# Kernel optimization log

Measured on AMD Instinct MI355X. Metric: run time of the kernel, lower is better.

The kernel has to match this reference:

```python
import jax, jax.numpy as jnp
import numpy as np

B, S, D, H = 4, 2048, 2048, 8192  # batch, seq, d_model, hidden (power of 2 for FHT)


def fwht(x):
    """Fast Walsh-Hadamard transform along the last axis, normalized by 1/sqrt(n).

    Iterative butterfly: O(n log n). n must be a power of 2.
    """
    orig_shape = x.shape
    n = orig_shape[-1]
    x = x.reshape(-1, n)
    h = 1
    while h < n:
        # view as (rows, n/(2h) blocks, 2 halves, h) and do the butterfly
        xb = x.reshape(-1, n // (2 * h), 2, h)
        a = xb[:, :, 0, :]
        b = xb[:, :, 1, :]
        x = jnp.stack([a + b, a - b], axis=2).reshape(-1, n)
        h *= 2
    scale = jnp.asarray(1.0 / np.sqrt(n), dtype=x.dtype)
    return (x * scale).reshape(orig_shape)


def setup_inputs() -> dict:
    key = jax.random.key(0)
    kx, k1, k2, k3 = jax.random.split(key, 4)
    x = jax.random.normal(kx, (B, S, D), dtype=jnp.float32)
    # nn.Linear weights: [out_features, in_features], no bias (Llama FFN style)
    W1 = jax.random.normal(k1, (H, D), dtype=jnp.float32) * (1.0 / np.sqrt(D))
    W2 = jax.random.normal(k2, (D, H), dtype=jnp.float32) * (1.0 / np.sqrt(H))
    W3 = jax.random.normal(k3, (H, D), dtype=jnp.float32) * (1.0 / np.sqrt(D))
    return {"x": x, "W1": W1, "W2": W2, "W3": W3}


def reference(x, W1, W2, W3):
    # w2( fht( silu(w1(x)) * w3(x) ) )
    up_gate = jnp.einsum("bsd,hd->bsh", x, W1)          # w1(x): [B,S,H]
    up_lin = jnp.einsum("bsd,hd->bsh", x, W3)           # w3(x): [B,S,H]
    hidden = jax.nn.silu(up_gate) * up_lin              # SwiGLU gate
    hidden = fwht(hidden)                               # fast Hadamard transform over H
    out = jnp.einsum("bsh,dh->bsd", hidden, W2)         # w2(.): [B,S,D]
    return out
```

## Files before the change

### kernel.cpp

```cpp
#include <hip/hip_runtime.h>

typedef __attribute__((ext_vector_type(8))) __bf16 bf16x8;
typedef __attribute__((ext_vector_type(4))) float f32x4;

#define GLOAD_LDS16(g, l)                                                     \
  __builtin_amdgcn_global_load_lds(                                           \
      (const __attribute__((address_space(1))) void*)(g),                     \
      (__attribute__((address_space(3))) void*)(l), 16, 0, 0)

#define BAR() __builtin_amdgcn_s_barrier()
#define SB0() __builtin_amdgcn_sched_barrier(0)
#define LGKM(n)                                                               \
  do {                                                                        \
    asm volatile("s_waitcnt lgkmcnt(" #n ")" ::: "memory");                   \
    SB0();                                                                    \
  } while (0)
#define VMCNT0() asm volatile("s_waitcnt vmcnt(0)" ::: "memory")
#define PRIO1() __builtin_amdgcn_s_setprio(1)
#define PRIO0() __builtin_amdgcn_s_setprio(0)

__device__ __forceinline__ unsigned short f32_to_bf16(float f) {
  unsigned int u = __builtin_bit_cast(unsigned int, f);
  u += 0x7FFFu + ((u >> 16) & 1u);
  return (unsigned short)(u >> 16);
}

__global__ void conv_f32_bf16(const float* __restrict__ in,
                              unsigned short* __restrict__ out, int n4) {
  int stride = gridDim.x * blockDim.x;
  for (int i = blockIdx.x * blockDim.x + threadIdx.x; i < n4; i += stride) {
    float4 v = reinterpret_cast<const float4*>(in)[i];
    ushort4 o;
    o.x = f32_to_bf16(v.x);
    o.y = f32_to_bf16(v.y);
    o.z = f32_to_bf16(v.z);
    o.w = f32_to_bf16(v.w);
    reinterpret_cast<ushort4*>(out)[i] = o;
  }
}

__global__ void fwht_rows_bf16(const float* __restrict__ in,
                               unsigned short* __restrict__ out) {
  __shared__ float s[8192];
  const int tid = threadIdx.x;
  const float* row = in + (size_t)blockIdx.x * 8192;
#pragma unroll
  for (int i = 0; i < 8; ++i)
    reinterpret_cast<float4*>(s)[tid + i * 256] =
        reinterpret_cast<const float4*>(row)[tid + i * 256];
  for (int h = 1; h < 8192; h <<= 1) {
    __syncthreads();
#pragma unroll
    for (int it = 0; it < 16; ++it) {
      int i = tid + it * 256;
      int j = ((i & ~(h - 1)) << 1) | (i & (h - 1));
      float a = s[j], b = s[j + h];
      s[j] = a + b;
      s[j + h] = a - b;
    }
  }
  __syncthreads();
  const float scale = 0.011048543456039806f;
  unsigned short* orow = out + (size_t)blockIdx.x * 8192;
#pragma unroll
  for (int i = 0; i < 8; ++i) {
    float4 v = reinterpret_cast<const float4*>(s)[tid + i * 256];
    ushort4 o;
    o.x = f32_to_bf16(v.x * scale);
    o.y = f32_to_bf16(v.y * scale);
    o.z = f32_to_bf16(v.z * scale);
    o.w = f32_to_bf16(v.w * scale);
    reinterpret_cast<ushort4*>(orow)[tid + i * 256] = o;
  }
}

#define MFMA_BF16 __builtin_amdgcn_mfma_f32_16x16x32_bf16

#define G2_TILE(BI, tt)                                                       \
  {                                                                           \
    _Pragma("unroll") for (int m = 0; m < 4; ++m) {                           \
      ra[m][0] = *(const bf16x8*)(Lb + ((BI)*32768 + m * 2048) + rA0);        \
      ra[m][1] = *(const bf16x8*)(Lb + ((BI)*32768 + m * 2048) + rA1);        \
    }                                                                         \
    _Pragma("unroll") for (int n = 0; n < 2; ++n) {                           \
      rb[n][0] = *(const bf16x8*)(Lb + ((BI)*32768 + n * 2048) + rB0);        \
      rb[n][1] = *(const bf16x8*)(Lb + ((BI)*32768 + n * 2048) + rB1);        \
    }                                                                         \
    SB0();                                                                    \
    _Pragma("unroll") for (int n = 2; n < 4; ++n) {                           \
      rb[n][0] = *(const bf16x8*)(Lb + ((BI)*32768 + n * 2048) + rB0);        \
      rb[n][1] = *(const bf16x8*)(Lb + ((BI)*32768 + n * 2048) + rB1);        \
    }                                                                         \
    SB0();                                                                    \
    if ((tt) + 1 < NT) {                                                      \
      unsigned short* dA = L + (((BI) ^ 1) * 16384) + wid * 512;              \
      unsigned short* dB = L + 32768 + (((BI) ^ 1) * 16384) + wid * 512;      \
      _Pragma("unroll") for (int i = 0; i < 4; ++i) {                         \
        GLOAD_LDS16(pA + i * s64, dA + i * 4096);                             \
        GLOAD_LDS16(pB + i * s64, dB + i * 4096);                             \
      }                                                                       \
    }                                                                         \
    SB0();                                                                    \
    LGKM(4);                                                                  \
    PRIO1();                                                                  \
    _Pragma("unroll") for (int m = 0; m < 4; ++m)                             \
        _Pragma("unroll") for (int n = 0; n < 2; ++n) {                       \
      acc[m][n] = MFMA_BF16(ra[m][0], rb[n][0], acc[m][n], 0, 0, 0);          \
      acc[m][n] = MFMA_BF16(ra[m][1], rb[n][1], acc[m][n], 0, 0, 0);          \
    }                                                                         \
    PRIO0();                                                                  \
    SB0();                                                                    \
    LGKM(0);                                                                  \
    PRIO1();                                                                  \
    _Pragma("unroll") for (int m = 0; m < 4; ++m)                             \
        _Pragma("unroll") for (int n = 2; n < 4; ++n) {                       \
      acc[m][n] = MFMA_BF16(ra[m][0], rb[n][0], acc[m][n], 0, 0, 0);          \
      acc[m][n] = MFMA_BF16(ra[m][1], rb[n][1], acc[m][n], 0, 0, 0);          \
    }                                                                         \
    PRIO0();                                                                  \
    SB0();                                                                    \
    _Pragma("unroll") for (int m = 0; m < 4; ++m) {                           \
      ra[m][0] = *(const bf16x8*)(Lb + ((BI)*32768 + (m + 4) * 2048) + rA0);  \
      ra[m][1] = *(const bf16x8*)(Lb + ((BI)*32768 + (m + 4) * 2048) + rA1);  \
    }                                                                         \
    SB0();                                                                    \
    LGKM(0);                                                                  \
    PRIO1();                                                                  \
    _Pragma("unroll") for (int m = 0; m < 4; ++m)                             \
        _Pragma("unroll") for (int n = 2; n < 4; ++n) {                       \
      acc[4 + m][n] = MFMA_BF16(ra[m][0], rb[n][0], acc[4 + m][n], 0, 0, 0);  \
      acc[4 + m][n] = MFMA_BF16(ra[m][1], rb[n][1], acc[4 + m][n], 0, 0, 0);  \
    }                                                                         \
    _Pragma("unroll") for (int m = 0; m < 4; ++m)                             \
        _Pragma("unroll") for (int n = 0; n < 2; ++n) {                       \
      acc[4 + m][n] = MFMA_BF16(ra[m][0], rb[n][0], acc[4 + m][n], 0, 0, 0);  \
      acc[4 + m][n] = MFMA_BF16(ra[m][1], rb[n][1], acc[4 + m][n], 0, 0, 0);  \
    }                                                                         \
    PRIO0();                                                                  \
    VMCNT0();                                                                 \
    BAR();                                                                    \
    pA += 128;                                                                \
    pB += 128;                                                                \
  }

__launch_bounds__(512, 2)
__global__ void gemm2_pipe(const unsigned short* __restrict__ A,
                           const unsigned short* __restrict__ Bt,
                           float* __restrict__ C, int M, int N, int K) {
  __shared__ __align__(16) unsigned short L[65536];
  const int tid = threadIdx.x, lane = tid & 63, wid = tid >> 6;
  const int wr = wid >> 2, wc = wid & 3;
  const int nbx = N >> 8;
  const int cpx = (int)gridDim.x >> 3;
  const int swz = ((int)blockIdx.x & 7) * cpx + ((int)blockIdx.x >> 3);
  const int bm = (swz / nbx) << 8, bn = (swz % nbx) << 8;
  const int NT = K >> 6;

  const int lp0 = (lane & 15) * 128 + (((lane >> 4) << 4) ^ ((lane & 7) << 4));
  const int lp1 =
      (lane & 15) * 128 + ((64 | ((lane >> 4) << 4)) ^ ((lane & 7) << 4));
  const int rA0 = wr * 16384 + lp0, rA1 = wr * 16384 + lp1;
  const int rB0 = 65536 + wc * 8192 + lp0, rB1 = 65536 + wc * 8192 + lp1;

  const int swzc = ((lane & 7) ^ (lane >> 3)) << 4;
  const char* pA = (const char*)A +
                   ((size_t)(bm + (wid << 3) + (lane >> 3)) * K) * 2 + swzc;
  const char* pB = (const char*)Bt +
                   ((size_t)(bn + (wid << 3) + (lane >> 3)) * K) * 2 + swzc;
  const size_t s64 = (size_t)K * 128;
  const char* Lb = (const char*)L;

  {
    unsigned short* dA = L + wid * 512;
    unsigned short* dB = L + 32768 + wid * 512;
#pragma unroll
    for (int i = 0; i < 4; ++i) {
      GLOAD_LDS16(pA + i * s64, dA + i * 4096);
      GLOAD_LDS16(pB + i * s64, dB + i * 4096);
    }
  }
  pA += 128;
  pB += 128;

  f32x4 acc[8][4];
#pragma unroll
  for (int m = 0; m < 8; ++m)
#pragma unroll
    for (int n = 0; n < 4; ++n) acc[m][n] = (f32x4)0.0f;
  bf16x8 ra[4][2], rb[4][2];

  VMCNT0();
  BAR();

  for (int t = 0; t < NT; t += 2) {
    G2_TILE(0, t)
    G2_TILE(1, t + 1)
  }

  const int er = (lane >> 4) << 2;
  const int ec = lane & 15;
#pragma unroll
  for (int mi = 0; mi < 8; ++mi)
#pragma unroll
    for (int n = 0; n < 4; ++n)
#pragma unroll
      for (int r = 0; r < 4; ++r) {
        size_t row = (size_t)(bm + wr * 128 + mi * 16 + er + r);
        size_t col = (size_t)(bn + wc * 64 + n * 16 + ec);
        C[row * N + col] = acc[mi][n][r];
      }
}

#define G1_TILE(BI, tt)                                                       \
  {                                                                           \
    _Pragma("unroll") for (int m = 0; m < 4; ++m) {                           \
      ra[m][0] = *(const bf16x8*)(Lb + ((BI)*32768 + m * 2048) + rA0);        \
      ra[m][1] = *(const bf16x8*)(Lb + ((BI)*32768 + m * 2048) + rA1);        \
    }                                                                         \
    _Pragma("unroll") for (int n = 0; n < 2; ++n) {                           \
      rb[n][0] = *(const bf16x8*)(Lb + ((BI)*16384 + n * 2048) + rB0);        \
      rb[n][1] = *(const bf16x8*)(Lb + ((BI)*16384 + n * 2048) + rB1);        \
    }                                                                         \
    SB0();                                                                    \
    _Pragma("unroll") for (int n = 2; n < 4; ++n) {                           \
      rb[n][0] = *(const bf16x8*)(Lb + ((BI)*16384 + n * 2048) + rB0);        \
      rb[n][1] = *(const bf16x8*)(Lb + ((BI)*16384 + n * 2048) + rB1);        \
    }                                                                         \
    SB0();                                                                    \
    if ((tt) + 1 < NT) {                                                      \
      unsigned short* dA = L + (((BI) ^ 1) * 16384) + wid * 512;              \
      unsigned short* dB1 = L + 32768 + (((BI) ^ 1) * 8192) + wid * 512;      \
      unsigned short* dB3 = L + 49152 + (((BI) ^ 1) * 8192) + wid * 512;      \
      _Pragma("unroll") for (int i = 0; i < 4; ++i)                           \
          GLOAD_LDS16(pA + i * s64, dA + i * 4096);                           \
      _Pragma("unroll") for (int i = 0; i < 2; ++i) {                         \
        GLOAD_LDS16(pB1 + i * s64, dB1 + i * 4096);                           \
        GLOAD_LDS16(pB3 + i * s64, dB3 + i * 4096);                           \
      }                                                                       \
    }                                                                         \
    SB0();                                                                    \
    LGKM(4);                                                                  \
    PRIO1();                                                                  \
    _Pragma("unroll") for (int m = 0; m < 4; ++m)                             \
        _Pragma("unroll") for (int n = 0; n < 2; ++n) {                       \
      accG[m][n] = MFMA_BF16(ra[m][0], rb[n][0], accG[m][n], 0, 0, 0);        \
      accG[m][n] = MFMA_BF16(ra[m][1], rb[n][1], accG[m][n], 0, 0, 0);        \
    }                                                                         \
    PRIO0();                                                                  \
    SB0();                                                                    \
    LGKM(0);                                                                  \
    PRIO1();                                                                  \
    _Pragma("unroll") for (int m = 0; m < 4; ++m)                             \
        _Pragma("unroll") for (int n = 2; n < 4; ++n) {                       \
      accG[m][n] = MFMA_BF16(ra[m][0], rb[n][0], accG[m][n], 0, 0, 0);        \
      accG[m][n] = MFMA_BF16(ra[m][1], rb[n][1], accG[m][n], 0, 0, 0);        \
    }                                                                         \
    PRIO0();                                                                  \
    SB0();                                                                    \
    _Pragma("unroll") for (int n = 2; n < 4; ++n) {        \
      rb[n][0] = *(const bf16x8*)(Lb + (32768 + (BI)*16384 + n * 2048) + rB0);\
      rb[n][1] = *(const bf16x8*)(Lb + (32768 + (BI)*16384 + n * 2048) + rB1);\
    }                                                                         \
    SB0();                                                                    \
    _Pragma("unroll") for (int n = 0; n < 2; ++n) {                           \
      rb[n][0] = *(const bf16x8*)(Lb + (32768 + (BI)*16384 + n * 2048) + rB0);\
      rb[n][1] = *(const bf16x8*)(Lb + (32768 + (BI)*16384 + n * 2048) + rB1);\
    }                                                                         \
    SB0();                                                                    \
    LGKM(4);                                                                  \
    PRIO1();                                                                  \
    _Pragma("unroll") for (int m = 0; m < 4; ++m)                             \
        _Pragma("unroll") for (int n = 2; n < 4; ++n) {                       \
      accL[m][n] = MFMA_BF16(ra[m][0], rb[n][0], accL[m][n], 0, 0, 0);        \
      accL[m][n] = MFMA_BF16(ra[m][1], rb[n][1], accL[m][n], 0, 0, 0);        \
    }                                                                         \
    PRIO0();                                                                  \
    SB0();                                                                    \
    LGKM(0);                                                                  \
    PRIO1();                                                                  \
    _Pragma("unroll") for (int m = 0; m < 4; ++m)                             \
        _Pragma("unroll") for (int n = 0; n < 2; ++n) {                       \
      accL[m][n] = MFMA_BF16(ra[m][0], rb[n][0], accL[m][n], 0, 0, 0);        \
      accL[m][n] = MFMA_BF16(ra[m][1], rb[n][1], accL[m][n], 0, 0, 0);        \
    }                                                                         \
    PRIO0();                                                                  \
    VMCNT0();                                                                 \
    BAR();                                                                    \
    pA += 128;                                                                \
    pB1 += 128;                                                               \
    pB3 += 128;                                                               \
  }

__launch_bounds__(512, 2)
__global__ void gemm1_pipe(const unsigned short* __restrict__ A,
                           const unsigned short* __restrict__ B1p,
                           const unsigned short* __restrict__ B3p,
                           unsigned short* __restrict__ Hout, int M, int N,
                           int K) {
  __shared__ __align__(16) unsigned short L[65536];
  const int tid = threadIdx.x, lane = tid & 63, wid = tid >> 6;
  const int wr = wid >> 1, wc = wid & 1;
  const int nby = M >> 8;
  const int cpx = (int)gridDim.x >> 3;
  const int swz = ((int)blockIdx.x & 7) * cpx + ((int)blockIdx.x >> 3);
  const int bm = (swz % nby) << 8;
  const int bn = (swz / nby) << 7;
  const int NT = K >> 6;

  const int lp0 = (lane & 15) * 128 + (((lane >> 4) << 4) ^ ((lane & 7) << 4));
  const int lp1 =
      (lane & 15) * 128 + ((64 | ((lane >> 4) << 4)) ^ ((lane & 7) << 4));
  const int rA0 = wr * 8192 + lp0, rA1 = wr * 8192 + lp1;
  const int rB0 = 65536 + wc * 8192 + lp0, rB1 = 65536 + wc * 8192 + lp1;

  const int swzc = ((lane & 7) ^ (lane >> 3)) << 4;
  const char* pA = (const char*)A +
                   ((size_t)(bm + (wid << 3) + (lane >> 3)) * K) * 2 + swzc;
  const char* pB1 = (const char*)B1p +
                    ((size_t)(bn + (wid << 3) + (lane >> 3)) * K) * 2 + swzc;
  const char* pB3 = (const char*)B3p +
                    ((size_t)(bn + (wid << 3) + (lane >> 3)) * K) * 2 + swzc;
  const size_t s64 = (size_t)K * 128;
  const char* Lb = (const char*)L;

  {
    unsigned short* dA = L + wid * 512;
    unsigned short* dB1 = L + 32768 + wid * 512;
    unsigned short* dB3 = L + 49152 + wid * 512;
#pragma unroll
    for (int i = 0; i < 4; ++i) GLOAD_LDS16(pA + i * s64, dA + i * 4096);
#pragma unroll
    for (int i = 0; i < 2; ++i) {
      GLOAD_LDS16(pB1 + i * s64, dB1 + i * 4096);
      GLOAD_LDS16(pB3 + i * s64, dB3 + i * 4096);
    }
  }
  pA += 128;
  pB1 += 128;
  pB3 += 128;

  f32x4 accG[4][4], accL[4][4];
#pragma unroll
  for (int m = 0; m < 4; ++m)
#pragma unroll
    for (int n = 0; n < 4; ++n) {
      accG[m][n] = (f32x4)0.0f;
      accL[m][n] = (f32x4)0.0f;
    }
  bf16x8 ra[4][2], rb[4][2];

  VMCNT0();
  BAR();

  for (int t = 0; t < NT; t += 2) {
    G1_TILE(0, t)
    G1_TILE(1, t + 1)
  }

  const int er = (lane >> 4) << 2;
  const int ec = lane & 15;
#pragma unroll
  for (int m = 0; m < 4; ++m)
#pragma unroll
    for (int n = 0; n < 4; ++n)
#pragma unroll
      for (int r = 0; r < 4; ++r) {
        float g = accG[m][n][r];
        float li = accL[m][n][r];
        float h = (g / (1.0f + __expf(-g))) * li;
        size_t row = (size_t)(bm + wr * 64 + m * 16 + er + r);
        size_t col = (size_t)(bn + wc * 64 + n * 16 + ec);
        Hout[row * N + col] = f32_to_bf16(h);
      }
}

extern "C" void kernel_launch(void* const* d_in, const int* in_sizes, int n_in,
                              void* d_out, int out_size, void* d_ws,
                              size_t ws_size, hipStream_t stream) {
  const float* x = (const float*)d_in[0];
  const float* W1 = (const float*)d_in[1];
  const float* W2 = (const float*)d_in[2];
  const float* W3 = (const float*)d_in[3];
  float* out = (float*)d_out;

  const int M = 8192, D = 2048, H = 8192;
  const size_t NE = (size_t)16777216;

  unsigned short* xb = (unsigned short*)d_ws;
  unsigned short* w1b = xb + NE;
  unsigned short* w3b = w1b + NE;
  unsigned short* w2f = w3b + NE;
  unsigned short* hid = w2f + NE;

  conv_f32_bf16<<<2048, 256, 0, stream>>>(x, xb, (int)(NE / 4));
  conv_f32_bf16<<<2048, 256, 0, stream>>>(W1, w1b, (int)(NE / 4));
  conv_f32_bf16<<<2048, 256, 0, stream>>>(W3, w3b, (int)(NE / 4));
  fwht_rows_bf16<<<2048, 256, 0, stream>>>(W2, w2f);

  gemm1_pipe<<<(M / 256) * (H / 128), 512, 0, stream>>>(xb, w1b, w3b, hid, M,
                                                        H, D);
  gemm2_pipe<<<(M / 256) * (D / 256), 512, 0, stream>>>(hid, w2f, out, M, D,
                                                        H);
}
```

Measured before the change: 836.9 us.

## Shrink GEMM tiles to 4-wave blocks with K=32 stages for more occupancy

Both GEMMs are restructured from 512-thread blocks with 64-deep K tiles and 128KB of LDS to 256-thread blocks with 32-deep K tiles and 48KB of LDS. GEMM1 drops its M tile from 256 to 128 rows and GEMM2 drops its N tile from 256 to 128 columns, with a new LDS swizzle and load pattern. The aim is more resident blocks per CU, trading per-block data reuse for thread-level parallelism. In exchange, each pass over K needs twice as many barriers, and the smaller tiles mean more global and LDS traffic per flop.

```diff
diff --git a/kernel.cpp b/kernel.cpp
--- a/kernel.cpp
+++ b/kernel.cpp
@@ -18,6 +18,7 @@
 #define VMCNT0() asm volatile("s_waitcnt vmcnt(0)" ::: "memory")
 #define PRIO1() __builtin_amdgcn_s_setprio(1)
 #define PRIO0() __builtin_amdgcn_s_setprio(0)
+#define MFMA_BF16 __builtin_amdgcn_mfma_f32_16x16x32_bf16
 
 __device__ __forceinline__ unsigned short f32_to_bf16(float f) {
   unsigned int u = __builtin_bit_cast(unsigned int, f);
@@ -74,127 +75,95 @@
   }
 }
 
-#define MFMA_BF16 __builtin_amdgcn_mfma_f32_16x16x32_bf16
-
-#define G2_TILE(BI, tt)                                                       \
+#define G2T(BI, tt)                                                           \
   {                                                                           \
-    _Pragma("unroll") for (int m = 0; m < 4; ++m) {                           \
-      ra[m][0] = *(const bf16x8*)(Lb + ((BI)*32768 + m * 2048) + rA0);        \
-      ra[m][1] = *(const bf16x8*)(Lb + ((BI)*32768 + m * 2048) + rA1);        \
-    }                                                                         \
-    _Pragma("unroll") for (int n = 0; n < 2; ++n) {                           \
-      rb[n][0] = *(const bf16x8*)(Lb + ((BI)*32768 + n * 2048) + rB0);        \
-      rb[n][1] = *(const bf16x8*)(Lb + ((BI)*32768 + n * 2048) + rB1);        \
-    }                                                                         \
-    SB0();                                                                    \
-    _Pragma("unroll") for (int n = 2; n < 4; ++n) {                           \
-      rb[n][0] = *(const bf16x8*)(Lb + ((BI)*32768 + n * 2048) + rB0);        \
-      rb[n][1] = *(const bf16x8*)(Lb + ((BI)*32768 + n * 2048) + rB1);        \
-    }                                                                         \
+    _Pragma("unroll") for (int m = 0; m < 4; ++m) ra[m] =                     \
+        *(const bf16x8*)(Lb + (BI)*16384 + m * 1024 + aoff);                  \
+    _Pragma("unroll") for (int n = 0; n < 4; ++n) rb[n] =                     \
+        *(const bf16x8*)(Lb + 32768 + (BI)*8192 + n * 1024 + boff);           \
+    _Pragma("unroll") for (int m = 4; m < 8; ++m) ra[m] =                     \
+        *(const bf16x8*)(Lb + (BI)*16384 + m * 1024 + aoff);                  \
     SB0();                                                                    \
     if ((tt) + 1 < NT) {                                                      \
-      unsigned short* dA = L + (((BI) ^ 1) * 16384) + wid * 512;              \
-      unsigned short* dB = L + 32768 + (((BI) ^ 1) * 16384) + wid * 512;      \
-      _Pragma("unroll") for (int i = 0; i < 4; ++i) {                         \
-        GLOAD_LDS16(pA + i * s64, dA + i * 4096);                             \
-        GLOAD_LDS16(pB + i * s64, dB + i * 4096);                             \
-      }                                                                       \
+      unsigned short* dA = L + (((BI) ^ 1) * 8192) + wid * 2048;              \
+      unsigned short* dB = L + 16384 + (((BI) ^ 1) * 4096) + wid * 1024;      \
+      _Pragma("unroll") for (int i = 0; i < 4; ++i)                           \
+          GLOAD_LDS16(pA + i * s16, dA + i * 512);                            \
+      _Pragma("unroll") for (int i = 0; i < 2; ++i)                           \
+          GLOAD_LDS16(pB + i * s16, dB + i * 512);                            \
     }                                                                         \
     SB0();                                                                    \
     LGKM(4);                                                                  \
     PRIO1();                                                                  \
     _Pragma("unroll") for (int m = 0; m < 4; ++m)                             \
-        _Pragma("unroll") for (int n = 0; n < 2; ++n) {                       \
-      acc[m][n] = MFMA_BF16(ra[m][0], rb[n][0], acc[m][n], 0, 0, 0);          \
-      acc[m][n] = MFMA_BF16(ra[m][1], rb[n][1], acc[m][n], 0, 0, 0);          \
-    }                                                                         \
+        _Pragma("unroll") for (int n = 0; n < 4; ++n) acc[m][n] =             \
+            MFMA_BF16(ra[m], rb[n], acc[m][n], 0, 0, 0);                      \
     PRIO0();                                                                  \
     SB0();                                                                    \
     LGKM(0);                                                                  \
     PRIO1();                                                                  \
-    _Pragma("unroll") for (int m = 0; m < 4; ++m)                             \
-        _Pragma("unroll") for (int n = 2; n < 4; ++n) {                       \
-      acc[m][n] = MFMA_BF16(ra[m][0], rb[n][0], acc[m][n], 0, 0, 0);          \
-      acc[m][n] = MFMA_BF16(ra[m][1], rb[n][1], acc[m][n], 0, 0, 0);          \
-    }                                                                         \
-    PRIO0();                                                                  \
-    SB0();                                                                    \
-    _Pragma("unroll") for (int m = 0; m < 4; ++m) {                           \
-      ra[m][0] = *(const bf16x8*)(Lb + ((BI)*32768 + (m + 4) * 2048) + rA0);  \
-      ra[m][1] = *(const bf16x8*)(Lb + ((BI)*32768 + (m + 4) * 2048) + rA1);  \
-    }                                                                         \
-    SB0();                                                                    \
-    LGKM(0);                                                                  \
-    PRIO1();                                                                  \
-    _Pragma("unroll") for (int m = 0; m < 4; ++m)                             \
-        _Pragma("unroll") for (int n = 2; n < 4; ++n) {                       \
-      acc[4 + m][n] = MFMA_BF16(ra[m][0], rb[n][0], acc[4 + m][n], 0, 0, 0);  \
-      acc[4 + m][n] = MFMA_BF16(ra[m][1], rb[n][1], acc[4 + m][n], 0, 0, 0);  \
-    }                                                                         \
-    _Pragma("unroll") for (int m = 0; m < 4; ++m)                             \
-        _Pragma("unroll") for (int n = 0; n < 2; ++n) {                       \
-      acc[4 + m][n] = MFMA_BF16(ra[m][0], rb[n][0], acc[4 + m][n], 0, 0, 0);  \
-      acc[4 + m][n] = MFMA_BF16(ra[m][1], rb[n][1], acc[4 + m][n], 0, 0, 0);  \
-    }                                                                         \
+    _Pragma("unroll") for (int m = 4; m < 8; ++m)                             \
+        _Pragma("unroll") for (int n = 0; n < 4; ++n) acc[m][n] =             \
+            MFMA_BF16(ra[m], rb[n], acc[m][n], 0, 0, 0);                      \
     PRIO0();                                                                  \
     VMCNT0();                                                                 \
     BAR();                                                                    \
-    pA += 128;                                                                \
-    pB += 128;                                                                \
-  }
-
-__launch_bounds__(512, 2)
-__global__ void gemm2_pipe(const unsigned short* __restrict__ A,
-                           const unsigned short* __restrict__ Bt,
-                           float* __restrict__ C, int M, int N, int K) {
-  __shared__ __align__(16) unsigned short L[65536];
+    pA += 64;                                                                 \
+    pB += 64;                                                                 \
+  }
+
+__launch_bounds__(256, 2)
+__global__ void gemm2_tlp(const unsigned short* __restrict__ A,
+                          const unsigned short* __restrict__ Bt,
+                          float* __restrict__ C, int M, int N, int K) {
+  __shared__ __align__(16) unsigned short L[24576];
   const int tid = threadIdx.x, lane = tid & 63, wid = tid >> 6;
-  const int wr = wid >> 2, wc = wid & 3;
-  const int nbx = N >> 8;
+  const int wr = wid >> 1, wc = wid & 1;
+
+  const int nby = M >> 8;
   const int cpx = (int)gridDim.x >> 3;
   const int swz = ((int)blockIdx.x & 7) * cpx + ((int)blockIdx.x >> 3);
-  const int bm = (swz / nbx) << 8, bn = (swz % nbx) << 8;
-  const int NT = K >> 6;
-
-  const int lp0 = (lane & 15) * 128 + (((lane >> 4) << 4) ^ ((lane & 7) << 4));
-  const int lp1 =
-      (lane & 15) * 128 + ((64 | ((lane >> 4) << 4)) ^ ((lane & 7) << 4));
-  const int rA0 = wr * 16384 + lp0, rA1 = wr * 16384 + lp1;
-  const int rB0 = 65536 + wc * 8192 + lp0, rB1 = 65536 + wc * 8192 + lp1;
-
-  const int swzc = ((lane & 7) ^ (lane >> 3)) << 4;
-  const char* pA = (const char*)A +
-                   ((size_t)(bm + (wid << 3) + (lane >> 3)) * K) * 2 + swzc;
-  const char* pB = (const char*)Bt +
-                   ((size_t)(bn + (wid << 3) + (lane >> 3)) * K) * 2 + swzc;
-  const size_t s64 = (size_t)K * 128;
+  const int bm = (swz % nby) << 8;
+  const int bn = (swz / nby) << 7;
+  const int NT = K >> 5;
+
+  const int lp =
+      (lane & 15) * 64 + ((((lane >> 4) ^ ((lane >> 1) & 3))) << 4);
+  const int aoff = wr * 8192 + lp;
+  const int boff = wc * 4096 + lp;
+
+  const int colb = (((lane & 3) ^ ((lane >> 3) & 3)) << 4);
+  const char* pA =
+      (const char*)A + (size_t)(bm + wid * 64 + (lane >> 2)) * K * 2 + colb;
+  const char* pB =
+      (const char*)Bt + (size_t)(bn + wid * 32 + (lane >> 2)) * K * 2 + colb;
+  const size_t s16 = (size_t)K * 32;
   const char* Lb = (const char*)L;
 
   {
-    unsigned short* dA = L + wid * 512;
-    unsigned short* dB = L + 32768 + wid * 512;
-#pragma unroll
-    for (int i = 0; i < 4; ++i) {
-      GLOAD_LDS16(pA + i * s64, dA + i * 4096);
-      GLOAD_LDS16(pB + i * s64, dB + i * 4096);
-    }
-  }
-  pA += 128;
-  pB += 128;
+    unsigned short* dA = L + wid * 2048;
+    unsigned short* dB = L + 16384 + wid * 1024;
+#pragma unroll
+    for (int i = 0; i < 4; ++i) GLOAD_LDS16(pA + i * s16, dA + i * 512);
+#pragma unroll
+    for (int i = 0; i < 2; ++i) GLOAD_LDS16(pB + i * s16, dB + i * 512);
+  }
+  pA += 64;
+  pB += 64;
 
   f32x4 acc[8][4];
 #pragma unroll
   for (int m = 0; m < 8; ++m)
 #pragma unroll
     for (int n = 0; n < 4; ++n) acc[m][n] = (f32x4)0.0f;
-  bf16x8 ra[4][2], rb[4][2];
+  bf16x8 ra[8], rb[4];
 
   VMCNT0();
   BAR();
 
   for (int t = 0; t < NT; t += 2) {
-    G2_TILE(0, t)
-    G2_TILE(1, t + 1)
+    G2T(0, t)
+    G2T(1, t + 1)
   }
 
   const int er = (lane >> 4) << 2;
@@ -211,133 +180,92 @@
       }
 }
 
-#define G1_TILE(BI, tt)                                                       \
+#define G1T(BI, tt)                                                           \
   {                                                                           \
-    _Pragma("unroll") for (int m = 0; m < 4; ++m) {                           \
-      ra[m][0] = *(const bf16x8*)(Lb + ((BI)*32768 + m * 2048) + rA0);        \
-      ra[m][1] = *(const bf16x8*)(Lb + ((BI)*32768 + m * 2048) + rA1);        \
-    }                                                                         \
-    _Pragma("unroll") for (int n = 0; n < 2; ++n) {                           \
-      rb[n][0] = *(const bf16x8*)(Lb + ((BI)*16384 + n * 2048) + rB0);        \
-      rb[n][1] = *(const bf16x8*)(Lb + ((BI)*16384 + n * 2048) + rB1);        \
-    }                                                                         \
-    SB0();                                                                    \
-    _Pragma("unroll") for (int n = 2; n < 4; ++n) {                           \
-      rb[n][0] = *(const bf16x8*)(Lb + ((BI)*16384 + n * 2048) + rB0);        \
-      rb[n][1] = *(const bf16x8*)(Lb + ((BI)*16384 + n * 2048) + rB1);        \
-    }                                                                         \
+    _Pragma("unroll") for (int m = 0; m < 4; ++m) ra[m] =                     \
+        *(const bf16x8*)(Lb + (BI)*8192 + m * 1024 + aoff);                   \
+    _Pragma("unroll") for (int n = 0; n < 4; ++n) rb1[n] =                    \
+        *(const bf16x8*)(Lb + 16384 + (BI)*8192 + n * 1024 + boff);           \
+    _Pragma("unroll") for (int n = 0; n < 4; ++n) rb3[n] =                    \
+        *(const bf16x8*)(Lb + 32768 + (BI)*8192 + n * 1024 + boff);           \
     SB0();                                                                    \
     if ((tt) + 1 < NT) {                                                      \
-      unsigned short* dA = L + (((BI) ^ 1) * 16384) + wid * 512;              \
-      unsigned short* dB1 = L + 32768 + (((BI) ^ 1) * 8192) + wid * 512;      \
-      unsigned short* dB3 = L + 49152 + (((BI) ^ 1) * 8192) + wid * 512;      \
-      _Pragma("unroll") for (int i = 0; i < 4; ++i)                           \
-          GLOAD_LDS16(pA + i * s64, dA + i * 4096);                           \
+      unsigned short* dA = L + (((BI) ^ 1) * 4096) + wid * 1024;              \
+      unsigned short* dB1 = L + 8192 + (((BI) ^ 1) * 4096) + wid * 1024;      \
+      unsigned short* dB3 = L + 16384 + (((BI) ^ 1) * 4096) + wid * 1024;     \
       _Pragma("unroll") for (int i = 0; i < 2; ++i) {                         \
-        GLOAD_LDS16(pB1 + i * s64, dB1 + i * 4096);                           \
-        GLOAD_LDS16(pB3 + i * s64, dB3 + i * 4096);                           \
+        GLOAD_LDS16(pA + i * s16, dA + i * 512);                              \
+        GLOAD_LDS16(pB1 + i * s16, dB1 + i * 512);                            \
+        GLOAD_LDS16(pB3 + i * s16, dB3 + i * 512);                            \
       }                                                                       \
     }                                                                         \
     SB0();                                                                    \
     LGKM(4);                                                                  \
     PRIO1();                                                                  \
     _Pragma("unroll") for (int m = 0; m < 4; ++m)                             \
-        _Pragma("unroll") for (int n = 0; n < 2; ++n) {                       \
-      accG[m][n] = MFMA_BF16(ra[m][0], rb[n][0], accG[m][n], 0, 0, 0);        \
-      accG[m][n] = MFMA_BF16(ra[m][1], rb[n][1], accG[m][n], 0, 0, 0);        \
-    }                                                                         \
+        _Pragma("unroll") for (int n = 0; n < 4; ++n) accG[m][n] =            \
+            MFMA_BF16(ra[m], rb1[n], accG[m][n], 0, 0, 0);                    \
     PRIO0();                                                                  \
     SB0();                                                                    \
     LGKM(0);                                                                  \
     PRIO1();                                                                  \
     _Pragma("unroll") for (int m = 0; m < 4; ++m)                             \
-        _Pragma("unroll") for (int n = 2; n < 4; ++n) {                       \
-      accG[m][n] = MFMA_BF16(ra[m][0], rb[n][0], accG[m][n], 0, 0, 0);        \
-      accG[m][n] = MFMA_BF16(ra[m][1], rb[n][1], accG[m][n], 0, 0, 0);        \
-    }                                                                         \
-    PRIO0();                                                                  \
-    SB0();                                                                    \
-    _Pragma("unroll") for (int n = 2; n < 4; ++n) {        \
-      rb[n][0] = *(const bf16x8*)(Lb + (32768 + (BI)*16384 + n * 2048) + rB0);\
-      rb[n][1] = *(const bf16x8*)(Lb + (32768 + (BI)*16384 + n * 2048) + rB1);\
-    }                                                                         \
-    SB0();                                                                    \
-    _Pragma("unroll") for (int n = 0; n < 2; ++n) {                           \
-      rb[n][0] = *(const bf16x8*)(Lb + (32768 + (BI)*16384 + n * 2048) + rB0);\
-      rb[n][1] = *(const bf16x8*)(Lb + (32768 + (BI)*16384 + n * 2048) + rB1);\
-    }                                                                         \
-    SB0();                                                                    \
-    LGKM(4);                                                                  \
-    PRIO1();                                                                  \
-    _Pragma("unroll") for (int m = 0; m < 4; ++m)                             \
-        _Pragma("unroll") for (int n = 2; n < 4; ++n) {                       \
-      accL[m][n] = MFMA_BF16(ra[m][0], rb[n][0], accL[m][n], 0, 0, 0);        \
-      accL[m][n] = MFMA_BF16(ra[m][1], rb[n][1], accL[m][n], 0, 0, 0);        \
-    }                                                                         \
-    PRIO0();                                                                  \
-    SB0();                                                                    \
-    LGKM(0);                                                                  \
-    PRIO1();                                                                  \
-    _Pragma("unroll") for (int m = 0; m < 4; ++m)                             \
-        _Pragma("unroll") for (int n = 0; n < 2; ++n) {                       \
-      accL[m][n] = MFMA_BF16(ra[m][0], rb[n][0], accL[m][n], 0, 0, 0);        \
-      accL[m][n] = MFMA_BF16(ra[m][1], rb[n][1], accL[m][n], 0, 0, 0);        \
-    }                                                                         \
+        _Pragma("unroll") for (int n = 0; n < 4; ++n) accL[m][n] =            \
+            MFMA_BF16(ra[m], rb3[n], accL[m][n], 0, 0, 0);                    \
     PRIO0();                                                                  \
     VMCNT0();                                                                 \
     BAR();                                                                    \
-    pA += 128;                                                                \
-    pB1 += 128;                                                               \
-    pB3 += 128;                                                               \
-  }
-
-__launch_bounds__(512, 2)
-__global__ void gemm1_pipe(const unsigned short* __restrict__ A,
-                           const unsigned short* __restrict__ B1p,
-                           const unsigned short* __restrict__ B3p,
-                           unsigned short* __restrict__ Hout, int M, int N,
-                           int K) {
-  __shared__ __align__(16) unsigned short L[65536];
+    pA += 64;                                                                 \
+    pB1 += 64;                                                                \
+    pB3 += 64;                                                                \
+  }
+
+__launch_bounds__(256, 2)
+__global__ void gemm1_tlp(const unsigned short* __restrict__ A,
+                          const unsigned short* __restrict__ B1p,
+                          const unsigned short* __restrict__ B3p,
+                          unsigned short* __restrict__ Hout, int M, int N,
+                          int K) {
+  __shared__ __align__(16) unsigned short L[24576];
   const int tid = threadIdx.x, lane = tid & 63, wid = tid >> 6;
   const int wr = wid >> 1, wc = wid & 1;
-  const int nby = M >> 8;
+
+  const int nby = M >> 7;
   const int cpx = (int)gridDim.x >> 3;
   const int swz = ((int)blockIdx.x & 7) * cpx + ((int)blockIdx.x >> 3);
-  const int bm = (swz % nby) << 8;
+  const int bm = (swz % nby) << 7;
   const int bn = (swz / nby) << 7;
-  const int NT = K >> 6;
-
-  const int lp0 = (lane & 15) * 128 + (((lane >> 4) << 4) ^ ((lane & 7) << 4));
-  const int lp1 =
-      (lane & 15) * 128 + ((64 | ((lane >> 4) << 4)) ^ ((lane & 7) << 4));
-  const int rA0 = wr * 8192 + lp0, rA1 = wr * 8192 + lp1;
-  const int rB0 = 65536 + wc * 8192 + lp0, rB1 = 65536 + wc * 8192 + lp1;
-
-  const int swzc = ((lane & 7) ^ (lane >> 3)) << 4;
-  const char* pA = (const char*)A +
-                   ((size_t)(bm + (wid << 3) + (lane >> 3)) * K) * 2 + swzc;
-  const char* pB1 = (const char*)B1p +
-                    ((size_t)(bn + (wid << 3) + (lane >> 3)) * K) * 2 + swzc;
-  const char* pB3 = (const char*)B3p +
-                    ((size_t)(bn + (wid << 3) + (lane >> 3)) * K) * 2 + swzc;
-  const size_t s64 = (size_t)K * 128;
+  const int NT = K >> 5;
+
+  const int lp =
+      (lane & 15) * 64 + ((((lane >> 4) ^ ((lane >> 1) & 3))) << 4);
+  const int aoff = wr * 4096 + lp;
+  const int boff = wc * 4096 + lp;
+
+  const int colb = (((lane & 3) ^ ((lane >> 3) & 3)) << 4);
+  const char* pA =
+      (const char*)A + (size_t)(bm + wid * 32 + (lane >> 2)) * K * 2 + colb;
+  const char* pB1 =
+      (const char*)B1p + (size_t)(bn + wid * 32 + (lane >> 2)) * K * 2 + colb;
+  const char* pB3 =
+      (const char*)B3p + (size_t)(bn + wid * 32 + (lane >> 2)) * K * 2 + colb;
+  const size_t s16 = (size_t)K * 32;
   const char* Lb = (const char*)L;
 
   {
-    unsigned short* dA = L + wid * 512;
-    unsigned short* dB1 = L + 32768 + wid * 512;
-    unsigned short* dB3 = L + 49152 + wid * 512;
-#pragma unroll
-    for (int i = 0; i < 4; ++i) GLOAD_LDS16(pA + i * s64, dA + i * 4096);
+    unsigned short* dA = L + wid * 1024;
+    unsigned short* dB1 = L + 8192 + wid * 1024;
+    unsigned short* dB3 = L + 16384 + wid * 1024;
 #pragma unroll
     for (int i = 0; i < 2; ++i) {
-      GLOAD_LDS16(pB1 + i * s64, dB1 + i * 4096);
-      GLOAD_LDS16(pB3 + i * s64, dB3 + i * 4096);
+      GLOAD_LDS16(pA + i * s16, dA + i * 512);
+      GLOAD_LDS16(pB1 + i * s16, dB1 + i * 512);
+      GLOAD_LDS16(pB3 + i * s16, dB3 + i * 512);
     }
   }
-  pA += 128;
-  pB1 += 128;
-  pB3 += 128;
+  pA += 64;
+  pB1 += 64;
+  pB3 += 64;
 
   f32x4 accG[4][4], accL[4][4];
 #pragma unroll
@@ -347,14 +275,14 @@
       accG[m][n] = (f32x4)0.0f;
       accL[m][n] = (f32x4)0.0f;
     }
-  bf16x8 ra[4][2], rb[4][2];
+  bf16x8 ra[4], rb1[4], rb3[4];
 
   VMCNT0();
   BAR();
 
   for (int t = 0; t < NT; t += 2) {
-    G1_TILE(0, t)
-    G1_TILE(1, t + 1)
+    G1T(0, t)
+    G1T(1, t + 1)
   }
 
   const int er = (lane >> 4) << 2;
@@ -397,8 +325,8 @@
   conv_f32_bf16<<<2048, 256, 0, stream>>>(W3, w3b, (int)(NE / 4));
   fwht_rows_bf16<<<2048, 256, 0, stream>>>(W2, w2f);
 
-  gemm1_pipe<<<(M / 256) * (H / 128), 512, 0, stream>>>(xb, w1b, w3b, hid, M,
-                                                        H, D);
-  gemm2_pipe<<<(M / 256) * (D / 256), 512, 0, stream>>>(hid, w2f, out, M, D,
-                                                        H);
-}
+  gemm1_tlp<<<(M / 128) * (H / 128), 256, 0, stream>>>(xb, w1b, w3b, hid, M,
+                                                       H, D);
+  gemm2_tlp<<<(M / 256) * (D / 128), 256, 0, stream>>>(hid, w2f, out, M, D,
+                                                       H);
+}
```

Measured after the change: 1.115 ms. +33.3%, slower.

## Switch both GEMMs from 16x16x32 to 32x32x16 bf16 MFMA tiles

Applied to the files above, without the earlier changes.

Both GEMM kernels now issue 32x32x16 bf16 MFMA instructions with 16-float accumulators instead of 16x16x32 with 4-float accumulators. The LDS read pattern and swizzle offsets are recomputed for the 32-row operand layout, and the epilogue row/column mapping is rewritten to match. Each operand fragment now feeds a larger output block, so fewer LDS fragment reads and MFMA issues are needed per tile. In exchange the inner schedule is simplified, with fewer waits and more fragment registers held live at once.

```diff
diff --git a/kernel.cpp b/kernel.cpp
--- a/kernel.cpp
+++ b/kernel.cpp
@@ -1,7 +1,7 @@
 #include <hip/hip_runtime.h>
 
 typedef __attribute__((ext_vector_type(8))) __bf16 bf16x8;
-typedef __attribute__((ext_vector_type(4))) float f32x4;
+typedef __attribute__((ext_vector_type(16))) float f32x16;
 
 #define GLOAD_LDS16(g, l)                                                     \
   __builtin_amdgcn_global_load_lds(                                           \
@@ -18,6 +18,7 @@
 #define VMCNT0() asm volatile("s_waitcnt vmcnt(0)" ::: "memory")
 #define PRIO1() __builtin_amdgcn_s_setprio(1)
 #define PRIO0() __builtin_amdgcn_s_setprio(0)
+#define MFMA32 __builtin_amdgcn_mfma_f32_32x32x16_bf16
 
 __device__ __forceinline__ unsigned short f32_to_bf16(float f) {
   unsigned int u = __builtin_bit_cast(unsigned int, f);
@@ -74,23 +75,19 @@
   }
 }
 
-#define MFMA_BF16 __builtin_amdgcn_mfma_f32_16x16x32_bf16
-
-#define G2_TILE(BI, tt)                                                       \
+#define G2T(BI, tt)                                                           \
   {                                                                           \
-    _Pragma("unroll") for (int m = 0; m < 4; ++m) {                           \
-      ra[m][0] = *(const bf16x8*)(Lb + ((BI)*32768 + m * 2048) + rA0);        \
-      ra[m][1] = *(const bf16x8*)(Lb + ((BI)*32768 + m * 2048) + rA1);        \
-    }                                                                         \
-    _Pragma("unroll") for (int n = 0; n < 2; ++n) {                           \
-      rb[n][0] = *(const bf16x8*)(Lb + ((BI)*32768 + n * 2048) + rB0);        \
-      rb[n][1] = *(const bf16x8*)(Lb + ((BI)*32768 + n * 2048) + rB1);        \
-    }                                                                         \
-    SB0();                                                                    \
-    _Pragma("unroll") for (int n = 2; n < 4; ++n) {                           \
-      rb[n][0] = *(const bf16x8*)(Lb + ((BI)*32768 + n * 2048) + rB0);        \
-      rb[n][1] = *(const bf16x8*)(Lb + ((BI)*32768 + n * 2048) + rB1);        \
-    }                                                                         \
+    _Pragma("unroll") for (int mi = 0; mi < 2; ++mi)                          \
+        _Pragma("unroll") for (int ks = 0; ks < 4; ++ks) ra[mi][ks] =         \
+            *(const bf16x8*)(Lb + (BI)*32768 + aB + mi * 4096 + sk[ks]);      \
+    _Pragma("unroll") for (int ni = 0; ni < 2; ++ni)                          \
+        _Pragma("unroll") for (int ks = 0; ks < 4; ++ks) rb[ni][ks] =         \
+            *(const bf16x8*)(Lb + 65536 + (BI)*32768 + bB + ni * 4096 +       \
+                             sk[ks]);                                         \
+    _Pragma("unroll") for (int mi = 0; mi < 2; ++mi)                          \
+        _Pragma("unroll") for (int ks = 0; ks < 4; ++ks) ra2[mi][ks] =        \
+            *(const bf16x8*)(Lb + (BI)*32768 + aB + 8192 + mi * 4096 +        \
+                             sk[ks]);                                         \
     SB0();                                                                    \
     if ((tt) + 1 < NT) {                                                      \
       unsigned short* dA = L + (((BI) ^ 1) * 16384) + wid * 512;              \
@@ -101,41 +98,21 @@
       }                                                                       \
     }                                                                         \
     SB0();                                                                    \
-    LGKM(4);                                                                  \
+    LGKM(8);                                                                  \
     PRIO1();                                                                  \
-    _Pragma("unroll") for (int m = 0; m < 4; ++m)                             \
-        _Pragma("unroll") for (int n = 0; n < 2; ++n) {                       \
-      acc[m][n] = MFMA_BF16(ra[m][0], rb[n][0], acc[m][n], 0, 0, 0);          \
-      acc[m][n] = MFMA_BF16(ra[m][1], rb[n][1], acc[m][n], 0, 0, 0);          \
-    }                                                                         \
+    _Pragma("unroll") for (int ks = 0; ks < 4; ++ks)                          \
+        _Pragma("unroll") for (int mi = 0; mi < 2; ++mi)                      \
+            _Pragma("unroll") for (int ni = 0; ni < 2; ++ni) acc[mi][ni] =    \
+                MFMA32(ra[mi][ks], rb[ni][ks], acc[mi][ni], 0, 0, 0);         \
     PRIO0();                                                                  \
     SB0();                                                                    \
     LGKM(0);                                                                  \
     PRIO1();                                                                  \
-    _Pragma("unroll") for (int m = 0; m < 4; ++m)                             \
-        _Pragma("unroll") for (int n = 2; n < 4; ++n) {                       \
-      acc[m][n] = MFMA_BF16(ra[m][0], rb[n][0], acc[m][n], 0, 0, 0);          \
-      acc[m][n] = MFMA_BF16(ra[m][1], rb[n][1], acc[m][n], 0, 0, 0);          \
-    }                                                                         \
-    PRIO0();                                                                  \
-    SB0();                                                                    \
-    _Pragma("unroll") for (int m = 0; m < 4; ++m) {                           \
-      ra[m][0] = *(const bf16x8*)(Lb + ((BI)*32768 + (m + 4) * 2048) + rA0);  \
-      ra[m][1] = *(const bf16x8*)(Lb + ((BI)*32768 + (m + 4) * 2048) + rA1);  \
-    }                                                                         \
-    SB0();                                                                    \
-    LGKM(0);                                                                  \
-    PRIO1();                                                                  \
-    _Pragma("unroll") for (int m = 0; m < 4; ++m)                             \
-        _Pragma("unroll") for (int n = 2; n < 4; ++n) {                       \
-      acc[4 + m][n] = MFMA_BF16(ra[m][0], rb[n][0], acc[4 + m][n], 0, 0, 0);  \
-      acc[4 + m][n] = MFMA_BF16(ra[m][1], rb[n][1], acc[4 + m][n], 0, 0, 0);  \
-    }                                                                         \
-    _Pragma("unroll") for (int m = 0; m < 4; ++m)                             \
-        _Pragma("unroll") for (int n = 0; n < 2; ++n) {                       \
-      acc[4 + m][n] = MFMA_BF16(ra[m][0], rb[n][0], acc[4 + m][n], 0, 0, 0);  \
-      acc[4 + m][n] = MFMA_BF16(ra[m][1], rb[n][1], acc[4 + m][n], 0, 0, 0);  \
-    }                                                                         \
+    _Pragma("unroll") for (int ks = 0; ks < 4; ++ks)                          \
+        _Pragma("unroll") for (int mi = 0; mi < 2; ++mi)                      \
+            _Pragma("unroll") for (int ni = 0; ni < 2; ++ni)                  \
+                acc[2 + mi][ni] =                                             \
+                    MFMA32(ra2[mi][ks], rb[ni][ks], acc[2 + mi][ni], 0, 0, 0);\
     PRIO0();                                                                  \
     VMCNT0();                                                                 \
     BAR();                                                                    \
@@ -144,9 +121,9 @@
   }
 
 __launch_bounds__(512, 2)
-__global__ void gemm2_pipe(const unsigned short* __restrict__ A,
-                           const unsigned short* __restrict__ Bt,
-                           float* __restrict__ C, int M, int N, int K) {
+__global__ void gemm2_32(const unsigned short* __restrict__ A,
+                         const unsigned short* __restrict__ Bt,
+                         float* __restrict__ C, int M, int N, int K) {
   __shared__ __align__(16) unsigned short L[65536];
   const int tid = threadIdx.x, lane = tid & 63, wid = tid >> 6;
   const int wr = wid >> 2, wc = wid & 3;
@@ -156,11 +133,12 @@
   const int bm = (swz / nbx) << 8, bn = (swz % nbx) << 8;
   const int NT = K >> 6;
 
-  const int lp0 = (lane & 15) * 128 + (((lane >> 4) << 4) ^ ((lane & 7) << 4));
-  const int lp1 =
-      (lane & 15) * 128 + ((64 | ((lane >> 4) << 4)) ^ ((lane & 7) << 4));
-  const int rA0 = wr * 16384 + lp0, rA1 = wr * 16384 + lp1;
-  const int rB0 = 65536 + wc * 8192 + lp0, rB1 = 65536 + wc * 8192 + lp1;
+  const int rl = lane & 31, kk = lane >> 5, rx = rl & 7;
+  int sk[4];
+#pragma unroll
+  for (int ks = 0; ks < 4; ++ks) sk[ks] = ((((ks << 1) | kk) ^ rx) << 4);
+  const int aB = wr * 16384 + rl * 128;
+  const int bB = wc * 8192 + rl * 128;
 
   const int swzc = ((lane & 7) ^ (lane >> 3)) << 4;
   const char* pA = (const char*)A +
@@ -182,50 +160,47 @@
   pA += 128;
   pB += 128;
 
-  f32x4 acc[8][4];
-#pragma unroll
-  for (int m = 0; m < 8; ++m)
-#pragma unroll
-    for (int n = 0; n < 4; ++n) acc[m][n] = (f32x4)0.0f;
-  bf16x8 ra[4][2], rb[4][2];
+  f32x16 acc[4][2];
+#pragma unroll
+  for (int m = 0; m < 4; ++m)
+#pragma unroll
+    for (int n = 0; n < 2; ++n) acc[m][n] = (f32x16)0.0f;
+  bf16x8 ra[2][4], rb[2][4], ra2[2][4];
 
   VMCNT0();
   BAR();
 
   for (int t = 0; t < NT; t += 2) {
-    G2_TILE(0, t)
-    G2_TILE(1, t + 1)
-  }
-
-  const int er = (lane >> 4) << 2;
-  const int ec = lane & 15;
-#pragma unroll
-  for (int mi = 0; mi < 8; ++mi)
-#pragma unroll
-    for (int n = 0; n < 4; ++n)
-#pragma unroll
-      for (int r = 0; r < 4; ++r) {
-        size_t row = (size_t)(bm + wr * 128 + mi * 16 + er + r);
-        size_t col = (size_t)(bn + wc * 64 + n * 16 + ec);
-        C[row * N + col] = acc[mi][n][r];
+    G2T(0, t)
+    G2T(1, t + 1)
+  }
+
+#pragma unroll
+  for (int mi = 0; mi < 4; ++mi)
+#pragma unroll
+    for (int ni = 0; ni < 2; ++ni)
+#pragma unroll
+      for (int e = 0; e < 16; ++e) {
+        size_t row = (size_t)(bm + wr * 128 + mi * 32 + (e & 3) +
+                              ((e >> 2) << 3) + (kk << 2));
+        size_t col = (size_t)(bn + wc * 64 + ni * 32 + rl);
+        C[row * N + col] = acc[mi][ni][e];
       }
 }
 
-#define G1_TILE(BI, tt)                                                       \
+#define G1T(BI, tt)                                                           \
   {                                                                           \
-    _Pragma("unroll") for (int m = 0; m < 4; ++m) {                           \
-      ra[m][0] = *(const bf16x8*)(Lb + ((BI)*32768 + m * 2048) + rA0);        \
-      ra[m][1] = *(const bf16x8*)(Lb + ((BI)*32768 + m * 2048) + rA1);        \
-    }                                                                         \
-    _Pragma("unroll") for (int n = 0; n < 2; ++n) {                           \
-      rb[n][0] = *(const bf16x8*)(Lb + ((BI)*16384 + n * 2048) + rB0);        \
-      rb[n][1] = *(const bf16x8*)(Lb + ((BI)*16384 + n * 2048) + rB1);        \
-    }                                                                         \
-    SB0();                                                                    \
-    _Pragma("unroll") for (int n = 2; n < 4; ++n) {                           \
-      rb[n][0] = *(const bf16x8*)(Lb + ((BI)*16384 + n * 2048) + rB0);        \
-      rb[n][1] = *(const bf16x8*)(Lb + ((BI)*16384 + n * 2048) + rB1);        \
-    }                                                                         \
+    _Pragma("unroll") for (int mi = 0; mi < 2; ++mi)                          \
+        _Pragma("unroll") for (int ks = 0; ks < 4; ++ks) ra[mi][ks] =         \
+            *(const bf16x8*)(Lb + (BI)*32768 + aB + mi * 4096 + sk[ks]);      \
+    _Pragma("unroll") for (int ni = 0; ni < 2; ++ni)                          \
+        _Pragma("unroll") for (int ks = 0; ks < 4; ++ks) rb1[ni][ks] =        \
+            *(const bf16x8*)(Lb + 65536 + (BI)*16384 + bB + ni * 4096 +       \
+                             sk[ks]);                                         \
+    _Pragma("unroll") for (int ni = 0; ni < 2; ++ni)                          \
+        _Pragma("unroll") for (int ks = 0; ks < 4; ++ks) rb3[ni][ks] =        \
+            *(const bf16x8*)(Lb + 98304 + (BI)*16384 + bB + ni * 4096 +       \
+                             sk[ks]);                                         \
     SB0();                                                                    \
     if ((tt) + 1 < NT) {                                                      \
       unsigned short* dA = L + (((BI) ^ 1) * 16384) + wid * 512;              \
@@ -239,50 +214,20 @@
       }                                                                       \
     }                                                                         \
     SB0();                                                                    \
-    LGKM(4);                                                                  \
+    LGKM(8);                                                                  \
     PRIO1();                                                                  \
-    _Pragma("unroll") for (int m = 0; m < 4; ++m)                             \
-        _Pragma("unroll") for (int n = 0; n < 2; ++n) {                       \
-      accG[m][n] = MFMA_BF16(ra[m][0], rb[n][0], accG[m][n], 0, 0, 0);        \
-      accG[m][n] = MFMA_BF16(ra[m][1], rb[n][1], accG[m][n], 0, 0, 0);        \
-    }                                                                         \
+    _Pragma("unroll") for (int ks = 0; ks < 4; ++ks)                          \
+        _Pragma("unroll") for (int mi = 0; mi < 2; ++mi)                      \
+            _Pragma("unroll") for (int ni = 0; ni < 2; ++ni) accG[mi][ni] =   \
+                MFMA32(ra[mi][ks], rb1[ni][ks], accG[mi][ni], 0, 0, 0);       \
     PRIO0();                                                                  \
     SB0();                                                                    \
     LGKM(0);                                                                  \
     PRIO1();                                                                  \
-    _Pragma("unroll") for (int m = 0; m < 4; ++m)                             \
-        _Pragma("unroll") for (int n = 2; n < 4; ++n) {                       \
-      accG[m][n] = MFMA_BF16(ra[m][0], rb[n][0], accG[m][n], 0, 0, 0);        \
-      accG[m][n] = MFMA_BF16(ra[m][1], rb[n][1], accG[m][n], 0, 0, 0);        \
-    }                                                                         \
-    PRIO0();                                                                  \
-    SB0();                                                                    \
-    _Pragma("unroll") for (int n = 2; n < 4; ++n) {        \
-      rb[n][0] = *(const bf16x8*)(Lb + (32768 + (BI)*16384 + n * 2048) + rB0);\
-      rb[n][1] = *(const bf16x8*)(Lb + (32768 + (BI)*16384 + n * 2048) + rB1);\
-    }                                                                         \
-    SB0();                                                                    \
-    _Pragma("unroll") for (int n = 0; n < 2; ++n) {                           \
-      rb[n][0] = *(const bf16x8*)(Lb + (32768 + (BI)*16384 + n * 2048) + rB0);\
-      rb[n][1] = *(const bf16x8*)(Lb + (32768 + (BI)*16384 + n * 2048) + rB1);\
-    }                                                                         \
-    SB0();                                                                    \
-    LGKM(4);                                                                  \
-    PRIO1();                                                                  \
-    _Pragma("unroll") for (int m = 0; m < 4; ++m)                             \
-        _Pragma("unroll") for (int n = 2; n < 4; ++n) {                       \
-      accL[m][n] = MFMA_BF16(ra[m][0], rb[n][0], accL[m][n], 0, 0, 0);        \
-      accL[m][n] = MFMA_BF16(ra[m][1], rb[n][1], accL[m][n], 0, 0, 0);        \
-    }                                                                         \
-    PRIO0();                                                                  \
-    SB0();                                                                    \
-    LGKM(0);                                                                  \
-    PRIO1();                                                                  \
-    _Pragma("unroll") for (int m = 0; m < 4; ++m)                             \
-        _Pragma("unroll") for (int n = 0; n < 2; ++n) {                       \
-      accL[m][n] = MFMA_BF16(ra[m][0], rb[n][0], accL[m][n], 0, 0, 0);        \
-      accL[m][n] = MFMA_BF16(ra[m][1], rb[n][1], accL[m][n], 0, 0, 0);        \
-    }                                                                         \
+    _Pragma("unroll") for (int ks = 0; ks < 4; ++ks)                          \
+        _Pragma("unroll") for (int mi = 0; mi < 2; ++mi)                      \
+            _Pragma("unroll") for (int ni = 0; ni < 2; ++ni) accL[mi][ni] =   \
+                MFMA32(ra[mi][ks], rb3[ni][ks], accL[mi][ni], 0, 0, 0);       \
     PRIO0();                                                                  \
     VMCNT0();                                                                 \
     BAR();                                                                    \
@@ -292,11 +237,11 @@
   }
 
 __launch_bounds__(512, 2)
-__global__ void gemm1_pipe(const unsigned short* __restrict__ A,
-                           const unsigned short* __restrict__ B1p,
-                           const unsigned short* __restrict__ B3p,
-                           unsigned short* __restrict__ Hout, int M, int N,
-                           int K) {
+__global__ void gemm1_32(const unsigned short* __restrict__ A,
+                         const unsigned short* __restrict__ B1p,
+                         const unsigned short* __restrict__ B3p,
+                         unsigned short* __restrict__ Hout, int M, int N,
+                         int K) {
   __shared__ __align__(16) unsigned short L[65536];
   const int tid = threadIdx.x, lane = tid & 63, wid = tid >> 6;
   const int wr = wid >> 1, wc = wid & 1;
@@ -307,11 +252,12 @@
   const int bn = (swz / nby) << 7;
   const int NT = K >> 6;
 
-  const int lp0 = (lane & 15) * 128 + (((lane >> 4) << 4) ^ ((lane & 7) << 4));
-  const int lp1 =
-      (lane & 15) * 128 + ((64 | ((lane >> 4) << 4)) ^ ((lane & 7) << 4));
-  const int rA0 = wr * 8192 + lp0, rA1 = wr * 8192 + lp1;
-  const int rB0 = 65536 + wc * 8192 + lp0, rB1 = 65536 + wc * 8192 + lp1;
+  const int rl = lane & 31, kk = lane >> 5, rx = rl & 7;
+  int sk[4];
+#pragma unroll
+  for (int ks = 0; ks < 4; ++ks) sk[ks] = ((((ks << 1) | kk) ^ rx) << 4);
+  const int aB = wr * 8192 + rl * 128;
+  const int bB = wc * 8192 + rl * 128;
 
   const int swzc = ((lane & 7) ^ (lane >> 3)) << 4;
   const char* pA = (const char*)A +
@@ -339,37 +285,36 @@
   pB1 += 128;
   pB3 += 128;
 
-  f32x4 accG[4][4], accL[4][4];
-#pragma unroll
-  for (int m = 0; m < 4; ++m)
-#pragma unroll
-    for (int n = 0; n < 4; ++n) {
-      accG[m][n] = (f32x4)0.0f;
-      accL[m][n] = (f32x4)0.0f;
+  f32x16 accG[2][2], accL[2][2];
+#pragma unroll
+  for (int m = 0; m < 2; ++m)
+#pragma unroll
+    for (int n = 0; n < 2; ++n) {
+      accG[m][n] = (f32x16)0.0f;
+      accL[m][n] = (f32x16)0.0f;
     }
-  bf16x8 ra[4][2], rb[4][2];
+  bf16x8 ra[2][4], rb1[2][4], rb3[2][4];
 
   VMCNT0();
   BAR();
 
   for (int t = 0; t < NT; t += 2) {
-    G1_TILE(0, t)
-    G1_TILE(1, t + 1)
-  }
-
-  const int er = (lane >> 4) << 2;
-  const int ec = lane & 15;
-#pragma unroll
-  for (int m = 0; m < 4; ++m)
-#pragma unroll
-    for (int n = 0; n < 4; ++n)
-#pragma unroll
-      for (int r = 0; r < 4; ++r) {
-        float g = accG[m][n][r];
-        float li = accL[m][n][r];
+    G1T(0, t)
+    G1T(1, t + 1)
+  }
+
+#pragma unroll
+  for (int mi = 0; mi < 2; ++mi)
+#pragma unroll
+    for (int ni = 0; ni < 2; ++ni)
+#pragma unroll
+      for (int e = 0; e < 16; ++e) {
+        float g = accG[mi][ni][e];
+        float li = accL[mi][ni][e];
         float h = (g / (1.0f + __expf(-g))) * li;
-        size_t row = (size_t)(bm + wr * 64 + m * 16 + er + r);
-        size_t col = (size_t)(bn + wc * 64 + n * 16 + ec);
+        size_t row = (size_t)(bm + wr * 64 + mi * 32 + (e & 3) +
+                              ((e >> 2) << 3) + (kk << 2));
+        size_t col = (size_t)(bn + wc * 64 + ni * 32 + rl);
         Hout[row * N + col] = f32_to_bf16(h);
       }
 }
@@ -397,8 +342,7 @@
   conv_f32_bf16<<<2048, 256, 0, stream>>>(W3, w3b, (int)(NE / 4));
   fwht_rows_bf16<<<2048, 256, 0, stream>>>(W2, w2f);
 
-  gemm1_pipe<<<(M / 256) * (H / 128), 512, 0, stream>>>(xb, w1b, w3b, hid, M,
-                                                        H, D);
-  gemm2_pipe<<<(M / 256) * (D / 256), 512, 0, stream>>>(hid, w2f, out, M, D,
-                                                        H);
-}
+  gemm1_32<<<(M / 256) * (H / 128), 512, 0, stream>>>(xb, w1b, w3b, hid, M, H,
+                                                      D);
+  gemm2_32<<<(M / 256) * (D / 256), 512, 0, stream>>>(hid, w2f, out, M, D, H);
+}
```

Measured after the change: 1.247 ms. +49.0%, slower.
